# Kernel tuning notes

Measured on AMD Instinct MI355X. Metric: run time of the kernel, lower is better.

Reference implementation:

```python
import jax, jax.numpy as jnp
import numpy as np

B, N = 4, 2048
PARAM_G = 0.125       # recovery rate
VIRUS_DEATH = 8e-5    # disease-induced death rate


def setup_inputs() -> dict:
    key = jax.random.key(0)
    ks = jax.random.split(key, 7)
    return {
        "param_b": jax.random.uniform(ks[0], (B, N, 1), jnp.float32),
        "contact": jax.random.uniform(ks[1], (B, N, 1), jnp.float32),
        "mob": jax.random.uniform(ks[2], (B, N, N), jnp.float32),
        "SIR": jax.random.uniform(ks[3], (B, N, 4), jnp.float32),
        "sps": jax.random.uniform(ks[4], (B, N, N), jnp.float32),
        # original loads birth_china.npy / death_china.npy and divides by 365000
        "nature_birth": jax.random.uniform(ks[5], (N, 1), jnp.float32) / 365000.0,
        "nature_death": jax.random.uniform(ks[6], (N, 1), jnp.float32) / 365000.0,
    }


def reference(param_b, contact, mob, SIR, sps, nature_birth, nature_death):
    b, n = SIR.shape[0], SIR.shape[1]
    eye = jnp.eye(n, dtype=bool)
    # zero out diagonal (no self-mobility)
    F_nm = jnp.where(eye[None], 0.0, mob)            # [B,N,N]
    sps_m = jnp.where(eye[None], 0.0, sps)           # [B,N,N]
    # torch: P = F_nm / F_nm.sum(1).unsqueeze(2)  -> divide row i,col j by sum_k F[b,k,j] broadcast over last dim
    col_sum = F_nm.sum(axis=1)                       # [B,N]
    P = F_nm / col_sum[:, :, None]                   # [B,N,N]
    fai = F_nm.sum(axis=(1, 2))[:, None]             # [B,1]

    S = SIR[..., 0:1]
    I = SIR[..., 1:2]
    R = SIR[..., 2:3]
    I_sum = SIR[..., 3:4]
    pop = S + I + R                                  # [B,N,1]
    tau = pop.sum(axis=1)                            # [B,1]
    m = (fai / tau)[:, :, None]                      # [B,1,1] mobility rate (scalar per batch)

    birth = nature_birth[None]                       # [1,N,1]
    death = nature_death[None]                       # [1,N,1]

    I_new = S / pop * param_b * contact * I          # new infections

    # flux term: sum_j m * X[b,j] * P[b,i,j] == m * (P @ X), fused matvec instead of [B,N,N] broadcast
    flux = lambda X: m * jnp.matmul(P, X)            # [B,N,1]

    R_t = R + PARAM_G * I - death * R - m * R + flux(R)
    I_t = I + I_new - death * I - PARAM_G * I - VIRUS_DEATH * I - m * I + flux(I)
    S_t = S - I_new - death * S + birth * pop - m * S + flux(S)
    I_sum_t = I_sum + I_new

    R0 = param_b * contact / (death + PARAM_G + VIRUS_DEATH + m)
    W_arrive = param_b * contact - death - PARAM_G - VIRUS_DEATH

    Ht_SIR = jnp.concatenate([R0, I_new, S_t, I_t, R_t, I_sum_t], axis=-1)       # [B,N,6]
    arrive1 = jnp.concatenate(
        [W_arrive, jnp.broadcast_to(m, S.shape), I, pop], axis=-1)               # [B,N,4]
    arrive2 = jnp.stack([sps_m, P], axis=-1)                                     # [B,N,N,2]
    return Ht_SIR, arrive1, arrive2
```

## Files before the change

### kernel.cpp

```cpp
#include <hip/hip_runtime.h>

#define NN 2048
#define BB 4
#define PARAM_G 0.125f
#define VIRUS_DEATH 8e-5f

#define WS_FAI  8192
#define WS_TAU  8196
#define WS_ZERO_FLOATS 8200

__global__ __launch_bounds__(256) void k_colsum(const float* __restrict__ mob,
                                                const float* __restrict__ SIR,
                                                float* ws) {
    int t  = threadIdx.x;
    int i0 = blockIdx.x * 16;
    int j  = blockIdx.y * 1024 + t * 4;
    int b  = blockIdx.z;
    const float* base = mob + ((size_t)b * NN + i0) * NN + j;
    float4 acc = make_float4(0.f, 0.f, 0.f, 0.f);
    #pragma unroll
    for (int r = 0; r < 16; ++r) {
        float4 v = *(const float4*)(base + (size_t)r * NN);
        unsigned d = (unsigned)((i0 + r) - j);
        if (d < 4u) ((float*)&v)[d] = 0.0f;
        acc.x += v.x; acc.y += v.y; acc.z += v.z; acc.w += v.w;
    }
    atomicAdd(&ws[b * NN + j + 0], acc.x);
    atomicAdd(&ws[b * NN + j + 1], acc.y);
    atomicAdd(&ws[b * NN + j + 2], acc.z);
    atomicAdd(&ws[b * NN + j + 3], acc.w);
    float s = acc.x + acc.y + acc.z + acc.w;
    for (int off = 32; off; off >>= 1) s += __shfl_down(s, off);
    if ((t & 63) == 0) atomicAdd(&ws[WS_FAI + b], s);
    if (blockIdx.x == 0 && blockIdx.y == 0) {
        float accT = 0.f;
        #pragma unroll
        for (int k = 0; k < 8; ++k) {
            int n = k * 256 + t;
            float4 sv = *(const float4*)(SIR + ((size_t)b * NN + n) * 4);
            accT += sv.x + sv.y + sv.z;
        }
        for (int off = 32; off; off >>= 1) accT += __shfl_down(accT, off);
        __shared__ float red[4];
        if ((t & 63) == 0) red[t >> 6] = accT;
        __syncthreads();
        if (t == 0) ws[WS_TAU + b] = red[0] + red[1] + red[2] + red[3];
    }
}

__global__ __launch_bounds__(256) void k_main(const float* __restrict__ mob,
                                              const float* __restrict__ sps,
                                              const float* __restrict__ SIR,
                                              const float* __restrict__ param_b,
                                              const float* __restrict__ contact,
                                              const float* __restrict__ nb,
                                              const float* __restrict__ nd,
                                              const float* ws,
                                              float* __restrict__ out0,
                                              float* __restrict__ out1,
                                              float* __restrict__ out2) {
    __shared__ __align__(16) float sS[NN];
    __shared__ __align__(16) float sI[NN];
    __shared__ __align__(16) float sR[NN];
    int t = threadIdx.x;
    int b = blockIdx.y;
    for (int j = t; j < NN; j += 256) {
        float4 s = *(const float4*)(SIR + ((size_t)b * NN + j) * 4);
        sS[j] = s.x; sI[j] = s.y; sR[j] = s.z;
    }
    __syncthreads();

    int w = t >> 6, lane = t & 63;
    int i0 = blockIdx.x * 8;
    float m = ws[WS_FAI + b] / ws[WS_TAU + b];
    #pragma unroll
    for (int k = 0; k < 2; ++k) {
        int i = i0 + w + 4 * k;
        float invc = 1.0f / ws[b * NN + i];
        size_t rowoff = ((size_t)b * NN + i) * NN;
        const float* mrow = mob + rowoff;
        const float* srow = sps + rowoff;
        float* orow = out2 + rowoff * 2;
        float aS = 0.f, aI = 0.f, aR = 0.f;
        #pragma unroll 4
        for (int iter = 0; iter < 16; ++iter) {
            int j2 = iter * 128 + lane * 2;
            float2 mv = *(const float2*)(mrow + j2);
            float2 sv = *(const float2*)(srow + j2);
            unsigned d = (unsigned)(i - j2);
            if (d == 0u)      { mv.x = 0.f; sv.x = 0.f; }
            else if (d == 1u) { mv.y = 0.f; sv.y = 0.f; }
            float2 xS = *(const float2*)&sS[j2];
            float2 xI = *(const float2*)&sI[j2];
            float2 xR = *(const float2*)&sR[j2];
            aS += mv.x * xS.x + mv.y * xS.y;
            aI += mv.x * xI.x + mv.y * xI.y;
            aR += mv.x * xR.x + mv.y * xR.y;
            *(float4*)(orow + (size_t)j2 * 2) =
                make_float4(sv.x, mv.x * invc, sv.y, mv.y * invc);
        }
        for (int off = 32; off; off >>= 1) {
            aS += __shfl_down(aS, off);
            aI += __shfl_down(aI, off);
            aR += __shfl_down(aR, off);
        }
        if (lane == 0) {
            int g = b * NN + i;
            float4 sir = *(const float4*)(SIR + (size_t)g * 4);
            float S = sir.x, I = sir.y, R = sir.z, Isum = sir.w;
            float pb = param_b[g], ct = contact[g];
            float birth = nb[i], death = nd[i];
            float pop   = S + I + R;
            float pbc   = pb * ct;
            float I_new = S / pop * pbc * I;
            float fS = m * aS * invc, fI = m * aI * invc, fR = m * aR * invc;
            float R_t    = R + PARAM_G * I - death * R - m * R + fR;
            float I_t    = I + I_new - death * I - PARAM_G * I - VIRUS_DEATH * I
                             - m * I + fI;
            float S_t    = S - I_new - death * S + birth * pop - m * S + fS;
            float Isum_t = Isum + I_new;
            float R0     = pbc / (death + PARAM_G + VIRUS_DEATH + m);
            float W      = pbc - death - PARAM_G - VIRUS_DEATH;
            float* o0 = out0 + (size_t)g * 6;
            *(float2*)(o0 + 0) = make_float2(R0, I_new);
            *(float2*)(o0 + 2) = make_float2(S_t, I_t);
            *(float2*)(o0 + 4) = make_float2(R_t, Isum_t);
            *(float4*)(out1 + (size_t)g * 4) = make_float4(W, m, I, pop);
        }
    }
}

extern "C" void kernel_launch(void* const* d_in, const int* in_sizes, int n_in,
                              void* d_out, int out_size, void* d_ws, size_t ws_size,
                              hipStream_t stream) {
    const float* param_b = (const float*)d_in[0];
    const float* contact = (const float*)d_in[1];
    const float* mob     = (const float*)d_in[2];
    const float* SIR     = (const float*)d_in[3];
    const float* sps     = (const float*)d_in[4];
    const float* nb      = (const float*)d_in[5];
    const float* nd      = (const float*)d_in[6];

    float* out  = (float*)d_out;
    float* out0 = out;
    float* out1 = out + (size_t)BB * NN * 6;
    float* out2 = out1 + (size_t)BB * NN * 4;
    float* ws   = (float*)d_ws;

    (void)hipMemsetAsync(ws, 0, (size_t)WS_ZERO_FLOATS * sizeof(float), stream);

    k_colsum<<<dim3(128, 2, BB), 256, 0, stream>>>(mob, SIR, ws);
    k_main  <<<dim3(NN / 8, BB), 256, 0, stream>>>(mob, sps, SIR, param_b, contact,
                                                   nb, nd, ws, out0, out1, out2);
}
```

Before: 312.3 us.

## Replace atomic column-sum with two-stage partial reduction and one-row-per-wave main kernel

Column sums of the masked mobility matrix are now written as per-block partials to workspace and reduced by a second small kernel, replacing roughly a million global float atomics and shrinking the memset. fai is derived from the reduced column sums. The main kernel now handles one row per wave with twice as many blocks, trading duplicated LDS staging of SIR for more parallelism. An extra kernel launch is added.

```diff
diff --git a/kernel.cpp b/kernel.cpp
--- a/kernel.cpp
+++ b/kernel.cpp
@@ -5,34 +5,45 @@
 #define PARAM_G 0.125f
 #define VIRUS_DEATH 8e-5f
 
-#define WS_FAI  8192
-#define WS_TAU  8196
-#define WS_ZERO_FLOATS 8200
+#define P_OFF   0
+#define CS_OFF  (32 * 8192)
+#define FAI_OFF (CS_OFF + 8192)
+#define TAU_OFF (FAI_OFF + 4)
 
-__global__ __launch_bounds__(256) void k_colsum(const float* __restrict__ mob,
-                                                const float* __restrict__ SIR,
-                                                float* ws) {
+__global__ __launch_bounds__(256) void k_colA(const float* __restrict__ mob,
+                                              float* __restrict__ ws) {
     int t  = threadIdx.x;
-    int i0 = blockIdx.x * 16;
+    int i0 = blockIdx.x * 64;
     int j  = blockIdx.y * 1024 + t * 4;
     int b  = blockIdx.z;
     const float* base = mob + ((size_t)b * NN + i0) * NN + j;
     float4 acc = make_float4(0.f, 0.f, 0.f, 0.f);
-    #pragma unroll
-    for (int r = 0; r < 16; ++r) {
+    #pragma unroll 16
+    for (int r = 0; r < 64; ++r) {
         float4 v = *(const float4*)(base + (size_t)r * NN);
         unsigned d = (unsigned)((i0 + r) - j);
         if (d < 4u) ((float*)&v)[d] = 0.0f;
         acc.x += v.x; acc.y += v.y; acc.z += v.z; acc.w += v.w;
     }
-    atomicAdd(&ws[b * NN + j + 0], acc.x);
-    atomicAdd(&ws[b * NN + j + 1], acc.y);
-    atomicAdd(&ws[b * NN + j + 2], acc.z);
-    atomicAdd(&ws[b * NN + j + 3], acc.w);
-    float s = acc.x + acc.y + acc.z + acc.w;
-    for (int off = 32; off; off >>= 1) s += __shfl_down(s, off);
-    if ((t & 63) == 0) atomicAdd(&ws[WS_FAI + b], s);
-    if (blockIdx.x == 0 && blockIdx.y == 0) {
+    *(float4*)(ws + P_OFF + blockIdx.x * 8192 + b * NN + j) = acc;
+}
+
+__global__ __launch_bounds__(256) void k_colB(const float* __restrict__ SIR,
+                                              float* ws) {
+    int t = threadIdx.x;
+    int g = blockIdx.x * 256 + t;
+    int b = g >> 11;
+    float s = 0.f;
+    #pragma unroll
+    for (int p = 0; p < 32; ++p) s += ws[P_OFF + p * 8192 + g];
+    ws[CS_OFF + g] = s;
+    float f = s;
+    for (int off = 32; off; off >>= 1) f += __shfl_down(f, off);
+    __shared__ float red[4];
+    if ((t & 63) == 0) red[t >> 6] = f;
+    __syncthreads();
+    if (t == 0) atomicAdd(&ws[FAI_OFF + b], red[0] + red[1] + red[2] + red[3]);
+    if ((blockIdx.x & 7) == 0) {
         float accT = 0.f;
         #pragma unroll
         for (int k = 0; k < 8; ++k) {
@@ -41,10 +52,10 @@
             accT += sv.x + sv.y + sv.z;
         }
         for (int off = 32; off; off >>= 1) accT += __shfl_down(accT, off);
-        __shared__ float red[4];
-        if ((t & 63) == 0) red[t >> 6] = accT;
+        __shared__ float red2[4];
+        if ((t & 63) == 0) red2[t >> 6] = accT;
         __syncthreads();
-        if (t == 0) ws[WS_TAU + b] = red[0] + red[1] + red[2] + red[3];
+        if (t == 0) ws[TAU_OFF + b] = red2[0] + red2[1] + red2[2] + red2[3];
     }
 }
 
@@ -55,7 +66,7 @@
                                               const float* __restrict__ contact,
                                               const float* __restrict__ nb,
                                               const float* __restrict__ nd,
-                                              const float* ws,
+                                              const float* __restrict__ ws,
                                               float* __restrict__ out0,
                                               float* __restrict__ out1,
                                               float* __restrict__ out2) {
@@ -71,62 +82,58 @@
     __syncthreads();
 
     int w = t >> 6, lane = t & 63;
-    int i0 = blockIdx.x * 8;
-    float m = ws[WS_FAI + b] / ws[WS_TAU + b];
-    #pragma unroll
-    for (int k = 0; k < 2; ++k) {
-        int i = i0 + w + 4 * k;
-        float invc = 1.0f / ws[b * NN + i];
-        size_t rowoff = ((size_t)b * NN + i) * NN;
-        const float* mrow = mob + rowoff;
-        const float* srow = sps + rowoff;
-        float* orow = out2 + rowoff * 2;
-        float aS = 0.f, aI = 0.f, aR = 0.f;
-        #pragma unroll 4
-        for (int iter = 0; iter < 16; ++iter) {
-            int j2 = iter * 128 + lane * 2;
-            float2 mv = *(const float2*)(mrow + j2);
-            float2 sv = *(const float2*)(srow + j2);
-            unsigned d = (unsigned)(i - j2);
-            if (d == 0u)      { mv.x = 0.f; sv.x = 0.f; }
-            else if (d == 1u) { mv.y = 0.f; sv.y = 0.f; }
-            float2 xS = *(const float2*)&sS[j2];
-            float2 xI = *(const float2*)&sI[j2];
-            float2 xR = *(const float2*)&sR[j2];
-            aS += mv.x * xS.x + mv.y * xS.y;
-            aI += mv.x * xI.x + mv.y * xI.y;
-            aR += mv.x * xR.x + mv.y * xR.y;
-            *(float4*)(orow + (size_t)j2 * 2) =
-                make_float4(sv.x, mv.x * invc, sv.y, mv.y * invc);
-        }
-        for (int off = 32; off; off >>= 1) {
-            aS += __shfl_down(aS, off);
-            aI += __shfl_down(aI, off);
-            aR += __shfl_down(aR, off);
-        }
-        if (lane == 0) {
-            int g = b * NN + i;
-            float4 sir = *(const float4*)(SIR + (size_t)g * 4);
-            float S = sir.x, I = sir.y, R = sir.z, Isum = sir.w;
-            float pb = param_b[g], ct = contact[g];
-            float birth = nb[i], death = nd[i];
-            float pop   = S + I + R;
-            float pbc   = pb * ct;
-            float I_new = S / pop * pbc * I;
-            float fS = m * aS * invc, fI = m * aI * invc, fR = m * aR * invc;
-            float R_t    = R + PARAM_G * I - death * R - m * R + fR;
-            float I_t    = I + I_new - death * I - PARAM_G * I - VIRUS_DEATH * I
-                             - m * I + fI;
-            float S_t    = S - I_new - death * S + birth * pop - m * S + fS;
-            float Isum_t = Isum + I_new;
-            float R0     = pbc / (death + PARAM_G + VIRUS_DEATH + m);
-            float W      = pbc - death - PARAM_G - VIRUS_DEATH;
-            float* o0 = out0 + (size_t)g * 6;
-            *(float2*)(o0 + 0) = make_float2(R0, I_new);
-            *(float2*)(o0 + 2) = make_float2(S_t, I_t);
-            *(float2*)(o0 + 4) = make_float2(R_t, Isum_t);
-            *(float4*)(out1 + (size_t)g * 4) = make_float4(W, m, I, pop);
-        }
+    int i = blockIdx.x * 4 + w;
+    float m    = ws[FAI_OFF + b] / ws[TAU_OFF + b];
+    float invc = 1.0f / ws[CS_OFF + b * NN + i];
+    size_t rowoff = ((size_t)b * NN + i) * NN;
+    const float* mrow = mob + rowoff;
+    const float* srow = sps + rowoff;
+    float* orow = out2 + rowoff * 2;
+    float aS = 0.f, aI = 0.f, aR = 0.f;
+    #pragma unroll 8
+    for (int iter = 0; iter < 16; ++iter) {
+        int j2 = iter * 128 + lane * 2;
+        float2 mv = *(const float2*)(mrow + j2);
+        float2 sv = *(const float2*)(srow + j2);
+        unsigned d = (unsigned)(i - j2);
+        if (d == 0u)      { mv.x = 0.f; sv.x = 0.f; }
+        else if (d == 1u) { mv.y = 0.f; sv.y = 0.f; }
+        float2 xS = *(const float2*)&sS[j2];
+        float2 xI = *(const float2*)&sI[j2];
+        float2 xR = *(const float2*)&sR[j2];
+        aS += mv.x * xS.x + mv.y * xS.y;
+        aI += mv.x * xI.x + mv.y * xI.y;
+        aR += mv.x * xR.x + mv.y * xR.y;
+        *(float4*)(orow + (size_t)j2 * 2) =
+            make_float4(sv.x, mv.x * invc, sv.y, mv.y * invc);
+    }
+    for (int off = 32; off; off >>= 1) {
+        aS += __shfl_down(aS, off);
+        aI += __shfl_down(aI, off);
+        aR += __shfl_down(aR, off);
+    }
+    if (lane == 0) {
+        int g = b * NN + i;
+        float4 sir = *(const float4*)(SIR + (size_t)g * 4);
+        float S = sir.x, I = sir.y, R = sir.z, Isum = sir.w;
+        float pb = param_b[g], ct = contact[g];
+        float birth = nb[i], death = nd[i];
+        float pop   = S + I + R;
+        float pbc   = pb * ct;
+        float I_new = S / pop * pbc * I;
+        float fS = m * aS * invc, fI = m * aI * invc, fR = m * aR * invc;
+        float R_t    = R + PARAM_G * I - death * R - m * R + fR;
+        float I_t    = I + I_new - death * I - PARAM_G * I - VIRUS_DEATH * I
+                         - m * I + fI;
+        float S_t    = S - I_new - death * S + birth * pop - m * S + fS;
+        float Isum_t = Isum + I_new;
+        float R0     = pbc / (death + PARAM_G + VIRUS_DEATH + m);
+        float W      = pbc - death - PARAM_G - VIRUS_DEATH;
+        float* o0 = out0 + (size_t)g * 6;
+        *(float2*)(o0 + 0) = make_float2(R0, I_new);
+        *(float2*)(o0 + 2) = make_float2(S_t, I_t);
+        *(float2*)(o0 + 4) = make_float2(R_t, Isum_t);
+        *(float4*)(out1 + (size_t)g * 4) = make_float4(W, m, I, pop);
     }
 }
 
@@ -147,9 +154,10 @@
     float* out2 = out1 + (size_t)BB * NN * 4;
     float* ws   = (float*)d_ws;
 
-    (void)hipMemsetAsync(ws, 0, (size_t)WS_ZERO_FLOATS * sizeof(float), stream);
+    (void)hipMemsetAsync(ws + FAI_OFF, 0, 4 * sizeof(float), stream);
 
-    k_colsum<<<dim3(128, 2, BB), 256, 0, stream>>>(mob, SIR, ws);
-    k_main  <<<dim3(NN / 8, BB), 256, 0, stream>>>(mob, sps, SIR, param_b, contact,
-                                                   nb, nd, ws, out0, out1, out2);
+    k_colA<<<dim3(32, 2, BB),  256, 0, stream>>>(mob, ws);
+    k_colB<<<32,               256, 0, stream>>>(SIR, ws);
+    k_main<<<dim3(NN / 4, BB), 256, 0, stream>>>(mob, sps, SIR, param_b, contact,
+                                                 nb, nd, ws, out0, out1, out2);
 }
```

Result: no change. 313.0 us (+0.2%).
